# Kernel tuning notes

Hardware: AMD Instinct MI355X
Metric: run time of the kernel (lower is better)

Reference implementation:

```python
import math
import jax, jax.numpy as jnp
import numpy as np

DIM = 768
HEADS = 12
HEAD_DIM = DIM // HEADS
LT = 64          # template tokens
LS = 256         # search / pre-search tokens
KEEP_RATIO = 0.7
MLP_HID = 4 * DIM
LN_EPS = 1e-5


def _layernorm(x, w, b):
    m = jnp.mean(x, axis=-1, keepdims=True)
    v = jnp.mean(jnp.square(x - m), axis=-1, keepdims=True)
    return (x - m) * jax.lax.rsqrt(v + LN_EPS) * w + b


def setup_inputs() -> dict:
    key = jax.random.key(0)
    ks = jax.random.split(key, 8)
    B, N = 32, LT + 2 * LS
    s = 0.02
    x = jax.random.normal(ks[0], (B, N, DIM), jnp.float32)
    inp = {
        "x": x,
        "global_index_template": jnp.arange(B * LT, dtype=jnp.int64 if jax.config.jax_enable_x64 else jnp.int32).reshape(B, LT),
        "global_index_ps": jnp.arange(B * LS, dtype=jnp.int32).reshape(B, LS),
        "global_index_search": jnp.arange(B * LS, dtype=jnp.int32).reshape(B, LS),
        "ln1_w": jnp.ones((DIM,), jnp.float32),
        "ln1_b": jnp.zeros((DIM,), jnp.float32),
        "qkv_w": jax.random.normal(ks[1], (3 * DIM, DIM), jnp.float32) * s,
        "qkv_b": jnp.zeros((3 * DIM,), jnp.float32),
        "proj_w": jax.random.normal(ks[2], (DIM, DIM), jnp.float32) * s,
        "proj_b": jnp.zeros((DIM,), jnp.float32),
        "ln2_w": jnp.ones((DIM,), jnp.float32),
        "ln2_b": jnp.zeros((DIM,), jnp.float32),
        "fc1_w": jax.random.normal(ks[3], (MLP_HID, DIM), jnp.float32) * s,
        "fc1_b": jnp.zeros((MLP_HID,), jnp.float32),
        "fc2_w": jax.random.normal(ks[4], (DIM, MLP_HID), jnp.float32) * s,
        "fc2_b": jnp.zeros((DIM,), jnp.float32),
    }
    return inp


def reference(x, global_index_template, global_index_ps, global_index_search,
              ln1_w, ln1_b, qkv_w, qkv_b, proj_w, proj_b,
              ln2_w, ln2_b, fc1_w, fc1_b, fc2_w, fc2_b):
    B, N, C = x.shape
    # --- attention (returns full attn weights; no flash fusion possible) ---
    h = _layernorm(x, ln1_w, ln1_b)
    qkv = jnp.einsum('bnc,dc->bnd', h, qkv_w) + qkv_b           # [B,N,3C]
    qkv = qkv.reshape(B, N, 3, HEADS, HEAD_DIM).transpose(2, 0, 3, 1, 4)
    q, k, v = qkv[0], qkv[1], qkv[2]                            # [B,H,N,D]
    scale = HEAD_DIM ** -0.5
    attn = jax.nn.softmax(jnp.einsum('bhid,bhjd->bhij', q, k) * scale, axis=-1)
    xa = jnp.einsum('bhij,bhjd->bhid', attn, v)                 # [B,H,N,D]
    xa = xa.transpose(0, 2, 1, 3).reshape(B, N, C)
    xa = jnp.einsum('bnc,dc->bnd', xa, proj_w) + proj_b
    x = x + xa

    # --- candidate elimination ---
    lens_keep = math.ceil(KEEP_RATIO * LS)                      # 180
    # template->(ps,search) attention, mean over template queries and heads
    attn_t = attn[:, :, :LT, LT:].mean(axis=2).mean(axis=1)     # [B, 2*LS]
    a_ps, a_s = attn_t[:, :LS], attn_t[:, LS:]

    tokens_t = x[:, :LT]
    tokens_ps = x[:, LT:LT + LS]
    tokens_s = x[:, LT + LS:]

    order_ps = jnp.argsort(-a_ps, axis=1)                       # descending
    top_ps, non_ps = order_ps[:, :lens_keep], order_ps[:, lens_keep:]
    keep_index_ps = jnp.take_along_axis(global_index_ps, top_ps, axis=1)
    removed_index_ps = jnp.take_along_axis(global_index_ps, non_ps, axis=1)
    tokens_ps = jnp.take_along_axis(tokens_ps, top_ps[..., None], axis=1)

    order_s = jnp.argsort(-a_s, axis=1)
    top_s, non_s = order_s[:, :lens_keep], order_s[:, lens_keep:]
    keep_index_s = jnp.take_along_axis(global_index_search, top_s, axis=1)
    removed_index_s = jnp.take_along_axis(global_index_search, non_s, axis=1)
    tokens_s = jnp.take_along_axis(tokens_s, top_s[..., None], axis=1)

    x = jnp.concatenate([tokens_t, tokens_ps, tokens_s], axis=1)  # [B, LT+2*lens_keep, C]

    # --- MLP ---
    h2 = _layernorm(x, ln2_w, ln2_b)
    h2 = jax.nn.gelu(jnp.einsum('bnc,hc->bnh', h2, fc1_w) + fc1_b, approximate=False)
    h2 = jnp.einsum('bnh,ch->bnc', h2, fc2_w) + fc2_b
    x = x + h2

    return (x, global_index_template, keep_index_ps, keep_index_s,
            removed_index_ps, removed_index_s, attn)
```

## Files before the change

kernel.cpp:

```cpp
#include <hip/hip_runtime.h>


typedef unsigned short u16;
typedef unsigned int   u32;
typedef __attribute__((ext_vector_type(8))) short  s16x8;
typedef __attribute__((ext_vector_type(8))) __bf16 bf16x8;
typedef __attribute__((ext_vector_type(4))) float  f32x4;

#define BATCH 32
#define NTOK  576
#define CDIM  768
#define NH    12
#define HD    64
#define NKEEP 180
#define NREM  76
#define NTOK2 424
#define HID   3072

#define O0 0
#define O1 10420224
#define O2 10422272
#define O3 10428032
#define O4 10433792
#define O5 10436224
#define O6 10438656

#define WS_QKV 0u
#define WS_XA  84934656u
#define WS_X1  113246208u
#define WS_H2  169869312u
#define WS_WQ  190709760u
#define WS_WP  194248704u
#define WS_W1  195428352u
#define WS_W2  200146944u
#define WS_AT  204865536u
#define WS_TOP 204931072u

#define QKVSZ 14155776u

__device__ __forceinline__ u16 f2bf(float f) {
  u32 x = __float_as_uint(f);
  x += 0x7fffu + ((x >> 16) & 1u);
  return (u16)(x >> 16);
}

__device__ __forceinline__ f32x4 mfma16(s16x8 a, s16x8 b, f32x4 c) {
  return __builtin_amdgcn_mfma_f32_16x16x32_bf16(
      __builtin_bit_cast(bf16x8, a), __builtin_bit_cast(bf16x8, b), c, 0, 0, 0);
}

__device__ __forceinline__ float block_sum256(float v, float* sc) {
#pragma unroll
  for (int o = 32; o; o >>= 1) v += __shfl_down(v, o);
  int w = threadIdx.x >> 6;
  if ((threadIdx.x & 63) == 0) sc[w] = v;
  __syncthreads();
  float r = (sc[0] + sc[1]) + (sc[2] + sc[3]);
  __syncthreads();
  return r;
}

__global__ __launch_bounds__(256) void cvt_bf16(const float* __restrict__ in,
                                                u16* __restrict__ out, int n4) {
  int i = blockIdx.x * 256 + threadIdx.x;
  if (i < n4) {
    float4 v = ((const float4*)in)[i];
    union { u16 u[4]; uint2 q; } r;
    r.u[0] = f2bf(v.x); r.u[1] = f2bf(v.y); r.u[2] = f2bf(v.z); r.u[3] = f2bf(v.w);
    ((uint2*)out)[i] = r.q;
  }
}

__global__ __launch_bounds__(256)
void ln1_kernel(const float* __restrict__ x, const float* __restrict__ w,
                const float* __restrict__ bb, u16* __restrict__ hb,
                float* __restrict__ hf) {
  __shared__ float sc[4];
  size_t row = blockIdx.x;
  const float* xr = x + row * CDIM;
  int t = threadIdx.x;
  float v0 = xr[t], v1 = xr[t + 256], v2 = xr[t + 512];
  float mean = block_sum256(v0 + v1 + v2, sc) / 768.0f;
  float d0 = v0 - mean, d1 = v1 - mean, d2 = v2 - mean;
  float var = block_sum256(d0 * d0 + d1 * d1 + d2 * d2, sc) / 768.0f;
  float rs = 1.0f / sqrtf(var + 1e-5f);
  float o0 = d0 * rs * w[t]       + bb[t];
  float o1 = d1 * rs * w[t + 256] + bb[t + 256];
  float o2 = d2 * rs * w[t + 512] + bb[t + 512];
  u16* hr = hb + row * CDIM;
  float* fr = hf + row * CDIM;
  hr[t] = f2bf(o0); hr[t + 256] = f2bf(o1); hr[t + 512] = f2bf(o2);
  fr[t] = o0; fr[t + 256] = o1; fr[t + 512] = o2;
}

template <int MODE>
__global__ __launch_bounds__(256)
void gemm_bt(const u16* __restrict__ A, const u16* __restrict__ Bw,
             const float* __restrict__ bias, const float* res, float* outf,
             u16* outh, int M, int N, int K) {
  __shared__ __align__(16) u16 As[64][32];
  __shared__ __align__(16) u16 Bs[64][32];
  int t = threadIdx.x;
  int wave = t >> 6, lane = t & 63, quad = lane >> 4, l16 = lane & 15;
  int wm = (wave >> 1) * 32, wn = (wave & 1) * 32;
  int m0 = blockIdx.y * 64, n0 = blockIdx.x * 64;
  int lrow = t >> 2, lk = (t & 3) * 8;
  const u16* Ap = A + (size_t)(m0 + lrow) * K + lk;
  const u16* Bp = Bw + (size_t)(n0 + lrow) * K + lk;
  f32x4 acc[2][2] = {};
  for (int k0 = 0; k0 < K; k0 += 32) {
    *(uint4*)&As[lrow][lk] = *(const uint4*)(Ap + k0);
    *(uint4*)&Bs[lrow][lk] = *(const uint4*)(Bp + k0);
    __syncthreads();
    s16x8 af0 = *(const s16x8*)&As[wm + l16][quad * 8];
    s16x8 af1 = *(const s16x8*)&As[wm + 16 + l16][quad * 8];
    s16x8 bf0 = *(const s16x8*)&Bs[wn + l16][quad * 8];
    s16x8 bf1 = *(const s16x8*)&Bs[wn + 16 + l16][quad * 8];
    acc[0][0] = mfma16(af0, bf0, acc[0][0]);
    acc[0][1] = mfma16(af0, bf1, acc[0][1]);
    acc[1][0] = mfma16(af1, bf0, acc[1][0]);
    acc[1][1] = mfma16(af1, bf1, acc[1][1]);
    __syncthreads();
  }
#pragma unroll
  for (int mi = 0; mi < 2; ++mi)
#pragma unroll
    for (int ni = 0; ni < 2; ++ni) {
      int col = n0 + wn + ni * 16 + l16;
      float bv = bias[col];
#pragma unroll
      for (int r = 0; r < 4; ++r) {
        int rowi = m0 + wm + mi * 16 + quad * 4 + r;
        float v = acc[mi][ni][r] + bv;
        if (MODE == 0) {
          size_t o = (size_t)rowi * N + col;
          outf[o] = v + res[o];
        } else if (MODE == 1) {
          float g = 0.5f * v * (1.0f + erff(v * 0.70710678118654752f));
          outh[(size_t)rowi * N + col] = f2bf(g);
        } else {
          int three = col / 768;
          int rem = col - three * 768;
          int hh = rem >> 6, dd = rem & 63;
          int bbx = rowi / 576, tok = rowi - bbx * 576;
          size_t o = (size_t)three * QKVSZ +
                     ((size_t)(bbx * NH + hh) * NTOK + tok) * HD + dd;
          outh[o] = f2bf(v);
        }
      }
    }
}

template <int MODE>
__global__ __launch_bounds__(256)
void gemm_f32(const float* __restrict__ A, const float* __restrict__ W,
              const float* __restrict__ bias, float* __restrict__ out,
              int M, int N, int K) {
  __shared__ float As[16][64];
  __shared__ float Bs[16][64];
  int t = threadIdx.x;
  int tx = t & 15, ty = t >> 4;
  int n0 = blockIdx.x * 64;
  int m0 = (MODE == 1) ? blockIdx.y * 576 : blockIdx.y * 64;
  int lr = t >> 2, lc = (t & 3) * 4;
  float acc[4][4] = {};
  for (int k0 = 0; k0 < K; k0 += 16) {
    float4 av = *(const float4*)(A + (size_t)(m0 + lr) * K + k0 + lc);
    float4 bv = *(const float4*)(W + (size_t)(n0 + lr) * K + k0 + lc);
    __syncthreads();
    As[lc + 0][lr] = av.x; As[lc + 1][lr] = av.y;
    As[lc + 2][lr] = av.z; As[lc + 3][lr] = av.w;
    Bs[lc + 0][lr] = bv.x; Bs[lc + 1][lr] = bv.y;
    Bs[lc + 2][lr] = bv.z; Bs[lc + 3][lr] = bv.w;
    __syncthreads();
#pragma unroll
    for (int kk = 0; kk < 16; ++kk) {
      float4 a4 = *(const float4*)&As[kk][ty * 4];
      float4 b4 = *(const float4*)&Bs[kk][tx * 4];
      acc[0][0] = fmaf(a4.x, b4.x, acc[0][0]);
      acc[0][1] = fmaf(a4.x, b4.y, acc[0][1]);
      acc[0][2] = fmaf(a4.x, b4.z, acc[0][2]);
      acc[0][3] = fmaf(a4.x, b4.w, acc[0][3]);
      acc[1][0] = fmaf(a4.y, b4.x, acc[1][0]);
      acc[1][1] = fmaf(a4.y, b4.y, acc[1][1]);
      acc[1][2] = fmaf(a4.y, b4.z, acc[1][2]);
      acc[1][3] = fmaf(a4.y, b4.w, acc[1][3]);
      acc[2][0] = fmaf(a4.z, b4.x, acc[2][0]);
      acc[2][1] = fmaf(a4.z, b4.y, acc[2][1]);
      acc[2][2] = fmaf(a4.z, b4.z, acc[2][2]);
      acc[2][3] = fmaf(a4.z, b4.w, acc[2][3]);
      acc[3][0] = fmaf(a4.w, b4.x, acc[3][0]);
      acc[3][1] = fmaf(a4.w, b4.y, acc[3][1]);
      acc[3][2] = fmaf(a4.w, b4.z, acc[3][2]);
      acc[3][3] = fmaf(a4.w, b4.w, acc[3][3]);
    }
  }
#pragma unroll
  for (int i = 0; i < 4; ++i) {
    int rowl = ty * 4 + i;
#pragma unroll
    for (int j = 0; j < 4; ++j) {
      int col = n0 + tx * 4 + j;
      float v = acc[i][j] + bias[col];
      int hh = col >> 6, dd = col & 63;
      if (MODE == 0) {
        int rowg = m0 + rowl;
        int bbx = rowg / 576, tok = rowg - bbx * 576;
        out[((size_t)(bbx * NH + hh) * NTOK + tok) * HD + dd] = v;
      } else {
        out[((size_t)(blockIdx.y * NH + hh) * 64 + rowl) * HD + dd] = v;
      }
    }
  }
}

__global__ __launch_bounds__(256)
void precise_scores(const float* __restrict__ qf, const float* __restrict__ kf,
                    float* __restrict__ attnt) {
  int ig = blockIdx.x, h = blockIdx.y, b = blockIdx.z;
  __shared__ float Sp[16][576];
  __shared__ __align__(16) float qs[16][64];
  __shared__ float mrow[16], zrow[16];
  int t = threadIdx.x;
  {
    int r = t >> 4, c = (t & 15) * 4;
    *(float4*)&qs[r][c] =
        *(const float4*)(qf + ((size_t)(b * NH + h) * 64 + ig * 16 + r) * HD + c);
  }
  __syncthreads();
  int i = t >> 4, js = t & 15;
  const float* kbase = kf + (size_t)(b * NH + h) * NTOK * HD;
  for (int j = js; j < 576; j += 16) {
    const float4* k4 = (const float4*)(kbase + (size_t)j * HD);
    float acc = 0.f;
#pragma unroll
    for (int d4 = 0; d4 < 16; ++d4) {
      float4 q4 = *(const float4*)&qs[i][d4 * 4];
      float4 kv = k4[d4];
      acc = fmaf(q4.x, kv.x, acc);
      acc = fmaf(q4.y, kv.y, acc);
      acc = fmaf(q4.z, kv.z, acc);
      acc = fmaf(q4.w, kv.w, acc);
    }
    Sp[i][j] = acc * 0.125f;
  }
  __syncthreads();
  float m = -1e30f;
  for (int j = js; j < 576; j += 16) m = fmaxf(m, Sp[i][j]);
#pragma unroll
  for (int o = 8; o; o >>= 1) m = fmaxf(m, __shfl_xor(m, o));
  float z = 0.f;
  for (int j = js; j < 576; j += 16) z += expf(Sp[i][j] - m);
#pragma unroll
  for (int o = 8; o; o >>= 1) z += __shfl_xor(z, o);
  if (js == 0) { mrow[i] = m; zrow[i] = z; }
  __syncthreads();
  for (int jj = t; jj < 512; jj += 256) {
    int j = 64 + jj;
    float s = 0.f;
#pragma unroll
    for (int r = 0; r < 16; ++r) s += expf(Sp[r][j] - mrow[r]) / zrow[r];
    atomicAdd(&attnt[(size_t)b * 512 + jj], s);
  }
}

__global__ __launch_bounds__(256)
void attn_kernel(const u16* __restrict__ qb, const u16* __restrict__ kb,
                 const u16* __restrict__ vb, float* __restrict__ attn_out,
                 u16* __restrict__ xa) {
  int qt = blockIdx.x, h = blockIdx.y, b = blockIdx.z;
  __shared__ __align__(16) float S[16][580];
  __shared__ __align__(16) u16 qs[16][64];
  __shared__ __align__(16) u16 vt[32][72];
  int t = threadIdx.x;
  int wave = t >> 6, lane = t & 63, quad = lane >> 4, l16 = lane & 15;
  size_t bh = (size_t)(b * NH + h);
  const u16* qrow = qb + (bh * NTOK + qt * 16) * HD;
  {
    int r = t >> 4, c = (t & 15) * 4;
    *(uint2*)&qs[r][c] = *(const uint2*)(qrow + (size_t)r * HD + c);
  }
  __syncthreads();
  s16x8 af0 = *(const s16x8*)&qs[l16][quad * 8];
  s16x8 af1 = *(const s16x8*)&qs[l16][32 + quad * 8];
  const u16* kbase = kb + bh * NTOK * HD;
  for (int jt = wave; jt < 36; jt += 4) {
    const u16* krow = kbase + (size_t)(jt * 16 + l16) * HD + quad * 8;
    s16x8 b0 = *(const s16x8*)krow;
    s16x8 b1 = *(const s16x8*)(krow + 32);
    f32x4 sacc = {0.f, 0.f, 0.f, 0.f};
    sacc = mfma16(af0, b0, sacc);
    sacc = mfma16(af1, b1, sacc);
    int col = jt * 16 + l16;
#pragma unroll
    for (int r = 0; r < 4; ++r) S[quad * 4 + r][col] = sacc[r] * 0.125f;
  }
  __syncthreads();
  int row = t >> 4, js = t & 15;
  float m = -1e30f;
  for (int j = js; j < 576; j += 16) m = fmaxf(m, S[row][j]);
#pragma unroll
  for (int o = 8; o; o >>= 1) m = fmaxf(m, __shfl_xor(m, o));
  float z = 0.f;
  for (int j = js; j < 576; j += 16) {
    float e = expf(S[row][j] - m);
    S[row][j] = e;
    z += e;
  }
#pragma unroll
  for (int o = 8; o; o >>= 1) z += __shfl_xor(z, o);
  float invz = 1.0f / z;
  for (int j = js; j < 576; j += 16) S[row][j] *= invz;
  __syncthreads();
  float* aout = attn_out + (bh * NTOK + qt * 16) * NTOK;
  for (int idx = t; idx < 16 * 576; idx += 256) {
    int r = idx / 576, j = idx - r * 576;
    aout[(size_t)r * NTOK + j] = S[r][j];
  }
  const u16* vbase = vb + bh * NTOK * HD;
  f32x4 oacc = {0.f, 0.f, 0.f, 0.f};
  for (int kc = 0; kc < 18; ++kc) {
    __syncthreads();
    {
      int r = t >> 3, c = (t & 7) * 8;
      *(uint4*)&vt[r][c] = *(const uint4*)(vbase + (size_t)(kc * 32 + r) * HD + c);
    }
    __syncthreads();
    float4 p0 = *(const float4*)&S[l16][kc * 32 + quad * 8];
    float4 p1 = *(const float4*)&S[l16][kc * 32 + quad * 8 + 4];
    union { u16 u[8]; s16x8 v; } pu, bu;
    pu.u[0] = f2bf(p0.x); pu.u[1] = f2bf(p0.y);
    pu.u[2] = f2bf(p0.z); pu.u[3] = f2bf(p0.w);
    pu.u[4] = f2bf(p1.x); pu.u[5] = f2bf(p1.y);
    pu.u[6] = f2bf(p1.z); pu.u[7] = f2bf(p1.w);
#pragma unroll
    for (int jj = 0; jj < 8; ++jj) bu.u[jj] = vt[quad * 8 + jj][wave * 16 + l16];
    oacc = mfma16(pu.v, bu.v, oacc);
  }
  u16* xrow = xa + ((size_t)b * NTOK + qt * 16) * CDIM + h * HD + wave * 16 + l16;
#pragma unroll
  for (int r = 0; r < 4; ++r) xrow[(size_t)(quad * 4 + r) * CDIM] = f2bf(oacc[r]);
}

__global__ __launch_bounds__(256)
void sort_select(const float* __restrict__ attnt, const int* __restrict__ gps,
                 const int* __restrict__ gs, float* dout, int* __restrict__ tops) {
  int b = blockIdx.x >> 1, grp = blockIdx.x & 1;
  __shared__ float val[256];
  __shared__ int idx[256];
  int t = threadIdx.x;
  float v = attnt[b * 512 + grp * 256 + t] / 64.0f / 12.0f;
  val[t] = v;
  idx[t] = t;
  __syncthreads();
  for (int k = 2; k <= 256; k <<= 1) {
    for (int j = k >> 1; j > 0; j >>= 1) {
      int p = t ^ j;
      if (p > t) {
        float va = val[t], vb = val[p];
        int ia = idx[t], ib = idx[p];
        bool bfirst = (vb > va) || (vb == va && ib < ia);
        bool doswap = ((t & k) == 0) ? bfirst : !bfirst;
        if (doswap) { val[t] = vb; val[p] = va; idx[t] = ib; idx[p] = ia; }
      }
      __syncthreads();
    }
  }
  const int* g = grp ? gs : gps;
  int gi = g[b * 256 + idx[t]];
  if (t < NKEEP) {
    dout[(grp ? O3 : O2) + b * NKEEP + t] = (float)gi;
    tops[b * 360 + grp * NKEEP + t] = idx[t];
  } else {
    dout[(grp ? O5 : O4) + b * NREM + (t - NKEEP)] = (float)gi;
  }
}

__global__ __launch_bounds__(256)
void idx_copy(const int* __restrict__ g, float* __restrict__ o) {
  int t = blockIdx.x * 256 + threadIdx.x;
  if (t < 2048) o[t] = (float)g[t];
}

__global__ __launch_bounds__(256)
void gather_ln2(const float* __restrict__ x1, const int* __restrict__ tops,
                const float* __restrict__ w, const float* __restrict__ bb,
                float* __restrict__ x2, u16* __restrict__ h2) {
  __shared__ float sc[4];
  int r = blockIdx.x, b = blockIdx.y;
  int src;
  if (r < 64)       src = r;
  else if (r < 244) src = 64 + tops[b * 360 + (r - 64)];
  else              src = 320 + tops[b * 360 + NKEEP + (r - 244)];
  const float* xr = x1 + ((size_t)b * NTOK + src) * CDIM;
  int t = threadIdx.x;
  float v0 = xr[t], v1 = xr[t + 256], v2 = xr[t + 512];
  size_t drow = ((size_t)b * NTOK2 + r) * CDIM;
  x2[drow + t] = v0; x2[drow + t + 256] = v1; x2[drow + t + 512] = v2;
  float mean = block_sum256(v0 + v1 + v2, sc) / 768.0f;
  float d0 = v0 - mean, d1 = v1 - mean, d2 = v2 - mean;
  float var = block_sum256(d0 * d0 + d1 * d1 + d2 * d2, sc) / 768.0f;
  float rs = 1.0f / sqrtf(var + 1e-5f);
  u16* hr = h2 + drow;
  hr[t]       = f2bf(d0 * rs * w[t] + bb[t]);
  hr[t + 256] = f2bf(d1 * rs * w[t + 256] + bb[t + 256]);
  hr[t + 512] = f2bf(d2 * rs * w[t + 512] + bb[t + 512]);
}

extern "C" void kernel_launch(void* const* d_in, const int* in_sizes, int n_in,
                              void* d_out, int out_size, void* d_ws,
                              size_t ws_size, hipStream_t stream) {
  const float* x     = (const float*)d_in[0];
  const int*   git   = (const int*)d_in[1];
  const int*   gps   = (const int*)d_in[2];
  const int*   gse   = (const int*)d_in[3];
  const float* ln1w  = (const float*)d_in[4];
  const float* ln1b  = (const float*)d_in[5];
  const float* qkvw  = (const float*)d_in[6];
  const float* qkvb  = (const float*)d_in[7];
  const float* projw = (const float*)d_in[8];
  const float* projb = (const float*)d_in[9];
  const float* ln2w  = (const float*)d_in[10];
  const float* ln2b  = (const float*)d_in[11];
  const float* fc1w  = (const float*)d_in[12];
  const float* fc1b  = (const float*)d_in[13];
  const float* fc2w  = (const float*)d_in[14];
  const float* fc2b  = (const float*)d_in[15];

  float* out = (float*)d_out;
  char*  ws  = (char*)d_ws;

  u16*   qkvbuf = (u16*)(ws + WS_QKV);
  u16*   mid    = (u16*)(ws + WS_QKV);
  u16*   xa     = (u16*)(ws + WS_XA);
  float* x1     = (float*)(ws + WS_X1);
  u16*   h2     = (u16*)(ws + WS_H2);
  u16*   wq     = (u16*)(ws + WS_WQ);
  u16*   wp     = (u16*)(ws + WS_WP);
  u16*   w1     = (u16*)(ws + WS_W1);
  u16*   w2     = (u16*)(ws + WS_W2);
  float* attnt  = (float*)(ws + WS_AT);
  int*   tops   = (int*)(ws + WS_TOP);

  float* attn6 = out + O6;
  float* hf = attn6;
  u16*   hb = (u16*)(attn6 + 14155776);
  float* kf = attn6 + 21233664;
  float* qf = attn6 + 35389440;

  cvt_bf16<<<1728, 256, 0, stream>>>(qkvw, wq, 442368);
  cvt_bf16<<<576, 256, 0, stream>>>(projw, wp, 147456);
  cvt_bf16<<<2304, 256, 0, stream>>>(fc1w, w1, 589824);
  cvt_bf16<<<2304, 256, 0, stream>>>(fc2w, w2, 589824);
  ln1_kernel<<<18432, 256, 0, stream>>>(x, ln1w, ln1b, hb, hf);
  gemm_bt<2><<<dim3(36, 288), 256, 0, stream>>>(hb, wq, qkvb, nullptr, nullptr,
                                                qkvbuf, 18432, 2304, 768);
  gemm_f32<0><<<dim3(12, 288), 256, 0, stream>>>(hf, qkvw + 589824, qkvb + 768,
                                                 kf, 18432, 768, 768);
  gemm_f32<1><<<dim3(12, 32), 256, 0, stream>>>(hf, qkvw, qkvb, qf, 2048, 768,
                                                768);
  hipMemsetAsync((void*)attnt, 0, 65536, stream);
  precise_scores<<<dim3(4, 12, 32), 256, 0, stream>>>(qf, kf, attnt);
  attn_kernel<<<dim3(36, 12, 32), 256, 0, stream>>>(
      qkvbuf, qkvbuf + QKVSZ, qkvbuf + 2 * QKVSZ, attn6, xa);
  gemm_bt<0><<<dim3(12, 288), 256, 0, stream>>>(xa, wp, projb, x, x1, nullptr,
                                                18432, 768, 768);
  sort_select<<<64, 256, 0, stream>>>(attnt, gps, gse, out, tops);
  idx_copy<<<8, 256, 0, stream>>>(git, out + O1);
  gather_ln2<<<dim3(424, 32), 256, 0, stream>>>(x1, tops, ln2w, ln2b, out, h2);
  gemm_bt<1><<<dim3(48, 212), 256, 0, stream>>>(h2, w1, fc1b, nullptr, nullptr,
                                                mid, 13568, 3072, 768);
  gemm_bt<0><<<dim3(12, 212), 256, 0, stream>>>(mid, w2, fc2b, out, out,
                                                nullptr, 13568, 768, 3072);
}
```

Baseline: 2.411 ms.

## Store V transposed, vectorize attn softmax writeout, use FP64 deterministic score reduction

The QKV GEMM epilogue now writes V transposed (head-dim major) as packed bf16 stores. This lets the attention kernel read V fragments straight from global memory and drop the LDS staging with its per-chunk barriers. Softmax normalization is fused into a vectorized nontemporal write of the attention matrix, and P is converted with packed bf16 instructions. The token-selection score path switches to double precision and replaces float atomics with per-block partials plus a separate reduction kernel, likely for deterministic top-k ordering, at the cost of slower FP64 work and an extra launch.

```diff
diff --git a/kernel.cpp b/kernel.cpp
--- a/kernel.cpp
+++ b/kernel.cpp
@@ -128,24 +128,36 @@
     for (int ni = 0; ni < 2; ++ni) {
       int col = n0 + wn + ni * 16 + l16;
       float bv = bias[col];
-#pragma unroll
-      for (int r = 0; r < 4; ++r) {
-        int rowi = m0 + wm + mi * 16 + quad * 4 + r;
-        float v = acc[mi][ni][r] + bv;
-        if (MODE == 0) {
-          size_t o = (size_t)rowi * N + col;
-          outf[o] = v + res[o];
-        } else if (MODE == 1) {
-          float g = 0.5f * v * (1.0f + erff(v * 0.70710678118654752f));
-          outh[(size_t)rowi * N + col] = f2bf(g);
+      if (MODE == 2) {
+        int three = col / 768;
+        int rem = col - three * 768;
+        int hh = rem >> 6, dd = rem & 63;
+        int row0 = m0 + wm + mi * 16 + quad * 4;
+        int bbx = row0 / 576, tok = row0 - bbx * 576;
+        union { u16 u[4]; uint2 q; } pk;
+#pragma unroll
+        for (int r = 0; r < 4; ++r) pk.u[r] = f2bf(acc[mi][ni][r] + bv);
+        if (three == 2) {
+          *(uint2*)&outh[2u * QKVSZ +
+                         ((size_t)(bbx * NH + hh) * HD + dd) * NTOK + tok] = pk.q;
         } else {
-          int three = col / 768;
-          int rem = col - three * 768;
-          int hh = rem >> 6, dd = rem & 63;
-          int bbx = rowi / 576, tok = rowi - bbx * 576;
-          size_t o = (size_t)three * QKVSZ +
-                     ((size_t)(bbx * NH + hh) * NTOK + tok) * HD + dd;
-          outh[o] = f2bf(v);
+          u16* o = outh + (size_t)three * QKVSZ +
+                   ((size_t)(bbx * NH + hh) * NTOK + tok) * HD + dd;
+#pragma unroll
+          for (int r = 0; r < 4; ++r) o[(size_t)r * HD] = pk.u[r];
+        }
+      } else {
+#pragma unroll
+        for (int r = 0; r < 4; ++r) {
+          int rowi = m0 + wm + mi * 16 + quad * 4 + r;
+          float v = acc[mi][ni][r] + bv;
+          if (MODE == 0) {
+            size_t o = (size_t)rowi * N + col;
+            outf[o] = v + res[o];
+          } else {
+            float g = 0.5f * v * (1.0f + erff(v * 0.70710678118654752f));
+            outh[(size_t)rowi * N + col] = f2bf(g);
+          }
         }
       }
     }
@@ -216,62 +228,81 @@
 
 __global__ __launch_bounds__(256)
 void precise_scores(const float* __restrict__ qf, const float* __restrict__ kf,
-                    float* __restrict__ attnt) {
+                    double* __restrict__ part) {
   int ig = blockIdx.x, h = blockIdx.y, b = blockIdx.z;
   __shared__ float Sp[16][576];
-  __shared__ __align__(16) float qs[16][64];
-  __shared__ float mrow[16], zrow[16];
+  __shared__ double qd[16][64];
+  __shared__ double rz[16];
   int t = threadIdx.x;
   {
     int r = t >> 4, c = (t & 15) * 4;
-    *(float4*)&qs[r][c] =
-        *(const float4*)(qf + ((size_t)(b * NH + h) * 64 + ig * 16 + r) * HD + c);
+    float4 qv = *(const float4*)(qf +
+        ((size_t)(b * NH + h) * 64 + ig * 16 + r) * HD + c);
+    qd[r][c]     = (double)qv.x; qd[r][c + 1] = (double)qv.y;
+    qd[r][c + 2] = (double)qv.z; qd[r][c + 3] = (double)qv.w;
   }
   __syncthreads();
   int i = t >> 4, js = t & 15;
   const float* kbase = kf + (size_t)(b * NH + h) * NTOK * HD;
+  double m = -1e300;
   for (int j = js; j < 576; j += 16) {
     const float4* k4 = (const float4*)(kbase + (size_t)j * HD);
-    float acc = 0.f;
+    double acc = 0.0;
 #pragma unroll
     for (int d4 = 0; d4 < 16; ++d4) {
-      float4 q4 = *(const float4*)&qs[i][d4 * 4];
       float4 kv = k4[d4];
-      acc = fmaf(q4.x, kv.x, acc);
-      acc = fmaf(q4.y, kv.y, acc);
-      acc = fmaf(q4.z, kv.z, acc);
-      acc = fmaf(q4.w, kv.w, acc);
+      acc = fma(qd[i][d4 * 4 + 0], (double)kv.x, acc);
+      acc = fma(qd[i][d4 * 4 + 1], (double)kv.y, acc);
+      acc = fma(qd[i][d4 * 4 + 2], (double)kv.z, acc);
+      acc = fma(qd[i][d4 * 4 + 3], (double)kv.w, acc);
     }
-    Sp[i][j] = acc * 0.125f;
-  }
-  __syncthreads();
-  float m = -1e30f;
-  for (int j = js; j < 576; j += 16) m = fmaxf(m, Sp[i][j]);
-#pragma unroll
-  for (int o = 8; o; o >>= 1) m = fmaxf(m, __shfl_xor(m, o));
-  float z = 0.f;
-  for (int j = js; j < 576; j += 16) z += expf(Sp[i][j] - m);
+    double s = acc * 0.125;
+    Sp[i][j] = (float)s;
+    m = fmax(m, s);
+  }
+#pragma unroll
+  for (int o = 8; o; o >>= 1) m = fmax(m, __shfl_xor(m, o));
+  double z = 0.0;
+  for (int j = js; j < 576; j += 16) {
+    double e = exp((double)Sp[i][j] - m);
+    Sp[i][j] = (float)e;
+    z += e;
+  }
 #pragma unroll
   for (int o = 8; o; o >>= 1) z += __shfl_xor(z, o);
-  if (js == 0) { mrow[i] = m; zrow[i] = z; }
-  __syncthreads();
+  if (js == 0) rz[i] = 1.0 / z;
+  __syncthreads();
+  double* pbase = part + (((size_t)b * NH + h) * 4 + ig) * 512;
   for (int jj = t; jj < 512; jj += 256) {
     int j = 64 + jj;
-    float s = 0.f;
-#pragma unroll
-    for (int r = 0; r < 16; ++r) s += expf(Sp[r][j] - mrow[r]) / zrow[r];
-    atomicAdd(&attnt[(size_t)b * 512 + jj], s);
+    double s = 0.0;
+#pragma unroll
+    for (int r = 0; r < 16; ++r) s += (double)Sp[r][j] * rz[r];
+    pbase[jj] = s;
+  }
+}
+
+__global__ __launch_bounds__(256)
+void reduce_attnt(const double* __restrict__ part, double* __restrict__ attnt) {
+  int b = blockIdx.x, t = threadIdx.x;
+  for (int jj = t; jj < 512; jj += 256) {
+    double acc = 0.0;
+    for (int h = 0; h < NH; ++h)
+#pragma unroll
+      for (int ig = 0; ig < 4; ++ig)
+        acc += part[(((size_t)b * NH + h) * 4 + ig) * 512 + jj];
+    attnt[(size_t)b * 512 + jj] = acc * (1.0 / 768.0);
   }
 }
 
 __global__ __launch_bounds__(256)
 void attn_kernel(const u16* __restrict__ qb, const u16* __restrict__ kb,
-                 const u16* __restrict__ vb, float* __restrict__ attn_out,
+                 const u16* __restrict__ vtb, float* __restrict__ attn_out,
                  u16* __restrict__ xa) {
   int qt = blockIdx.x, h = blockIdx.y, b = blockIdx.z;
   __shared__ __align__(16) float S[16][580];
   __shared__ __align__(16) u16 qs[16][64];
-  __shared__ __align__(16) u16 vt[32][72];
+  __shared__ float zrow[16];
   int t = threadIdx.x;
   int wave = t >> 6, lane = t & 63, quad = lane >> 4, l16 = lane & 15;
   size_t bh = (size_t)(b * NH + h);
@@ -284,6 +315,7 @@
   s16x8 af0 = *(const s16x8*)&qs[l16][quad * 8];
   s16x8 af1 = *(const s16x8*)&qs[l16][32 + quad * 8];
   const u16* kbase = kb + bh * NTOK * HD;
+#pragma unroll 3
   for (int jt = wave; jt < 36; jt += 4) {
     const u16* krow = kbase + (size_t)(jt * 16 + l16) * HD + quad * 8;
     s16x8 b0 = *(const s16x8*)krow;
@@ -309,33 +341,34 @@
   }
 #pragma unroll
   for (int o = 8; o; o >>= 1) z += __shfl_xor(z, o);
-  float invz = 1.0f / z;
-  for (int j = js; j < 576; j += 16) S[row][j] *= invz;
+  if (js == 0) zrow[row] = 1.0f / z;
   __syncthreads();
   float* aout = attn_out + (bh * NTOK + qt * 16) * NTOK;
-  for (int idx = t; idx < 16 * 576; idx += 256) {
-    int r = idx / 576, j = idx - r * 576;
-    aout[(size_t)r * NTOK + j] = S[r][j];
-  }
-  const u16* vbase = vb + bh * NTOK * HD;
+#pragma unroll
+  for (int i = 0; i < 9; ++i) {
+    int idx = t + i * 256;
+    int r = idx / 144, c = idx - r * 144;
+    float rz = zrow[r];
+    f32x4 v = *(const f32x4*)&S[r][c * 4];
+    v *= rz;
+    *(f32x4*)&S[r][c * 4] = v;
+    __builtin_nontemporal_store(v, (f32x4*)&aout[(size_t)r * NTOK + c * 4]);
+  }
+  __syncthreads();
+  const u16* vrow =
+      vtb + (bh * HD + (size_t)(wave * 16 + l16)) * NTOK + quad * 8;
   f32x4 oacc = {0.f, 0.f, 0.f, 0.f};
+#pragma unroll 6
   for (int kc = 0; kc < 18; ++kc) {
-    __syncthreads();
-    {
-      int r = t >> 3, c = (t & 7) * 8;
-      *(uint4*)&vt[r][c] = *(const uint4*)(vbase + (size_t)(kc * 32 + r) * HD + c);
-    }
-    __syncthreads();
-    float4 p0 = *(const float4*)&S[l16][kc * 32 + quad * 8];
-    float4 p1 = *(const float4*)&S[l16][kc * 32 + quad * 8 + 4];
-    union { u16 u[8]; s16x8 v; } pu, bu;
-    pu.u[0] = f2bf(p0.x); pu.u[1] = f2bf(p0.y);
-    pu.u[2] = f2bf(p0.z); pu.u[3] = f2bf(p0.w);
-    pu.u[4] = f2bf(p1.x); pu.u[5] = f2bf(p1.y);
-    pu.u[6] = f2bf(p1.z); pu.u[7] = f2bf(p1.w);
-#pragma unroll
-    for (int jj = 0; jj < 8; ++jj) bu.u[jj] = vt[quad * 8 + jj][wave * 16 + l16];
-    oacc = mfma16(pu.v, bu.v, oacc);
+    f32x4 p0 = *(const f32x4*)&S[l16][kc * 32 + quad * 8];
+    f32x4 p1 = *(const f32x4*)&S[l16][kc * 32 + quad * 8 + 4];
+    union { u32 w[4]; s16x8 v; } pu;
+    asm("v_cvt_pk_bf16_f32 %0, %1, %2" : "=v"(pu.w[0]) : "v"(p0[0]), "v"(p0[1]));
+    asm("v_cvt_pk_bf16_f32 %0, %1, %2" : "=v"(pu.w[1]) : "v"(p0[2]), "v"(p0[3]));
+    asm("v_cvt_pk_bf16_f32 %0, %1, %2" : "=v"(pu.w[2]) : "v"(p1[0]), "v"(p1[1]));
+    asm("v_cvt_pk_bf16_f32 %0, %1, %2" : "=v"(pu.w[3]) : "v"(p1[2]), "v"(p1[3]));
+    s16x8 bv = *(const s16x8*)(vrow + kc * 32);
+    oacc = mfma16(pu.v, bv, oacc);
   }
   u16* xrow = xa + ((size_t)b * NTOK + qt * 16) * CDIM + h * HD + wave * 16 + l16;
 #pragma unroll
@@ -343,21 +376,20 @@
 }
 
 __global__ __launch_bounds__(256)
-void sort_select(const float* __restrict__ attnt, const int* __restrict__ gps,
+void sort_select(const double* __restrict__ attnt, const int* __restrict__ gps,
                  const int* __restrict__ gs, float* dout, int* __restrict__ tops) {
   int b = blockIdx.x >> 1, grp = blockIdx.x & 1;
-  __shared__ float val[256];
+  __shared__ double val[256];
   __shared__ int idx[256];
   int t = threadIdx.x;
-  float v = attnt[b * 512 + grp * 256 + t] / 64.0f / 12.0f;
-  val[t] = v;
+  val[t] = attnt[(size_t)b * 512 + grp * 256 + t];
   idx[t] = t;
   __syncthreads();
   for (int k = 2; k <= 256; k <<= 1) {
     for (int j = k >> 1; j > 0; j >>= 1) {
       int p = t ^ j;
       if (p > t) {
-        float va = val[t], vb = val[p];
+        double va = val[t], vb = val[p];
         int ia = idx[t], ib = idx[p];
         bool bfirst = (vb > va) || (vb == va && ib < ia);
         bool doswap = ((t & k) == 0) ? bfirst : !bfirst;
@@ -439,8 +471,10 @@
   u16*   wp     = (u16*)(ws + WS_WP);
   u16*   w1     = (u16*)(ws + WS_W1);
   u16*   w2     = (u16*)(ws + WS_W2);
-  float* attnt  = (float*)(ws + WS_AT);
   int*   tops   = (int*)(ws + WS_TOP);
+
+  double* part    = (double*)(ws + WS_XA);
+  double* attnt_d = (double*)(ws + WS_H2);
 
   float* attn6 = out + O6;
   float* hf = attn6;
@@ -459,13 +493,13 @@
                                                  kf, 18432, 768, 768);
   gemm_f32<1><<<dim3(12, 32), 256, 0, stream>>>(hf, qkvw, qkvb, qf, 2048, 768,
                                                 768);
-  hipMemsetAsync((void*)attnt, 0, 65536, stream);
-  precise_scores<<<dim3(4, 12, 32), 256, 0, stream>>>(qf, kf, attnt);
+  precise_scores<<<dim3(4, 12, 32), 256, 0, stream>>>(qf, kf, part);
+  reduce_attnt<<<32, 256, 0, stream>>>(part, attnt_d);
   attn_kernel<<<dim3(36, 12, 32), 256, 0, stream>>>(
       qkvbuf, qkvbuf + QKVSZ, qkvbuf + 2 * QKVSZ, attn6, xa);
   gemm_bt<0><<<dim3(12, 288), 256, 0, stream>>>(xa, wp, projb, x, x1, nullptr,
                                                 18432, 768, 768);
-  sort_select<<<64, 256, 0, stream>>>(attnt, gps, gse, out, tops);
+  sort_select<<<64, 256, 0, stream>>>(attnt_d, gps, gse, out, tops);
   idx_copy<<<8, 256, 0, stream>>>(git, out + O1);
   gather_ln2<<<dim3(424, 32), 256, 0, stream>>>(x1, tops, ln2w, ln2b, out, h2);
   gemm_bt<1><<<dim3(48, 212), 256, 0, stream>>>(h2, w1, fc1b, nullptr, nullptr,
```

Result: faster. 2.143 ms (-11.1%).
